# Optimization experiments

Measured on AMD Instinct MI355X. Metric: run time of the kernel, lower is better.

Reference implementation:

```python
import jax, jax.numpy as jnp
import numpy as np

NUM_CODES = 4096
TEMPERATURE = 1.0
EPS = 1e-08


def setup_inputs() -> dict:
    key = jax.random.key(0)
    k1, k2, k3 = jax.random.split(key, 3)
    B, D, T = 16, 512, 1500
    encoder_stride = 320
    student_features = jax.random.normal(k1, (B, D, T), dtype=jnp.float32)
    codebook = jax.random.normal(k2, (NUM_CODES, D), dtype=jnp.float32)
    lengths = jax.random.randint(k3, (B,), 0, T * encoder_stride, dtype=jnp.int64)
    return {
        "student_features": student_features,
        "codebook": codebook,
        "lengths": lengths,
        "encoder_stride": encoder_stride,
    }


def _length_mask(lengths, T, stride):
    # frame t is valid iff t < floor(length / stride)  -> (B, T) float mask
    n_valid = jnp.minimum(lengths // stride, T)
    return (jnp.arange(T)[None, :] < n_valid[:, None]).astype(jnp.float32)


def reference(student_features, codebook, lengths, encoder_stride):
    B, D, T = student_features.shape
    mask = _length_mask(lengths, T, encoder_stride)            # (B, T)
    z = jnp.transpose(student_features, (0, 2, 1)).reshape(-1, D)  # (N, D), N = B*T
    # Euclidean cdist via ||z||^2 + ||c||^2 - 2 z c^T (same as torch.cdist GEMM path)
    z2 = jnp.sum(z * z, axis=-1, keepdims=True)                # (N, 1)
    c2 = jnp.sum(codebook * codebook, axis=-1)                 # (K,)
    d2 = z2 + c2[None, :] - 2.0 * (z @ codebook.T)             # (N, K)
    distances = jnp.sqrt(jnp.maximum(d2, 1e-12))
    logits = -distances / TEMPERATURE
    probs = jax.nn.softmax(logits, axis=-1)                    # (N, K)
    probs_masked = probs * mask.reshape(-1, 1)
    code_dist = jnp.sum(probs_masked, axis=0)                  # (K,)
    code_dist = code_dist / (jnp.sum(code_dist) + EPS)
    entropy = -jnp.sum(code_dist * jnp.log(code_dist + EPS))
    max_entropy = jnp.log(jnp.float32(NUM_CODES))
    return 1.0 - entropy / max_entropy
```

## Files before the change

kernel.cpp:

```cpp
#include <hip/hip_runtime.h>
#include <hip/hip_bf16.h>

#define NUM_B   16
#define DIM     512
#define TT      1500
#define NROWS   (NUM_B * TT)
#define NCODES  4096
#define ROW_TILES ((NROWS + 127) / 128)
#define NROWS_PAD (ROW_TILES * 128)
#define NSLICE  8
#define SHIFTC  30.0f
#define NBLKX   (NCODES / 128)
#define TBLKS   (NUM_B * 47)
#define CBLKS   (NCODES / 4)
#define NZERO   (NROWS_PAD + NSLICE * NCODES)
#define NZERO2  (NZERO + 1)
#define RPB     188

typedef __bf16 bf16x8 __attribute__((ext_vector_type(8)));
typedef float  floatx4 __attribute__((ext_vector_type(4)));
typedef unsigned short ushortx8 __attribute__((ext_vector_type(8)));

__device__ __forceinline__ void glds16(const void* g, void* l) {
    __builtin_amdgcn_global_load_lds(
        (__attribute__((address_space(1))) void*)(void*)g,
        (__attribute__((address_space(3))) void*)l, 16, 0, 0);
}

__global__ __launch_bounds__(256) void k_prep(
    const float* __restrict__ sf, const float* __restrict__ cb,
    unsigned short* __restrict__ zbf, unsigned short* __restrict__ cbbf,
    float* __restrict__ z2, float* __restrict__ c2, float* __restrict__ zero0,
    float* __restrict__ outp) {
    int id = blockIdx.x, tid = threadIdx.x;
    if (id < TBLKS) {
        __shared__ float tile[32][257];
        int b = id / 47, t0 = (id % 47) * 32;
        int tl = tid & 31, dg = tid >> 5;
        int tr = tid >> 3, dgr = tid & 7;
        int tg = t0 + tr;
        float ssq = 0.f;
        unsigned short* dst = zbf + (size_t)(b * TT + tg) * DIM;
#pragma unroll
        for (int half = 0; half < 2; ++half) {
            int dbase = half * 256;
            if (half) __syncthreads();
            int t = t0 + tl;
            if (t < TT) {
                const float* src = sf + (size_t)(b * DIM + dbase + dg * 32) * TT + t;
#pragma unroll
                for (int k = 0; k < 32; ++k)
                    tile[tl][dg * 32 + k] = src[(size_t)k * TT];
            }
            __syncthreads();
            if (tg < TT) {
#pragma unroll
                for (int seg = 0; seg < 4; ++seg) {
                    int d0 = seg * 64 + dgr * 8;
                    unsigned int h[8];
#pragma unroll
                    for (int i2 = 0; i2 < 8; ++i2) {
                        __hip_bfloat16 hb = __float2bfloat16(tile[tr][d0 + i2]);
                        h[i2] = __builtin_bit_cast(unsigned short, hb);
                        float vb = __bfloat162float(hb);
                        ssq += vb * vb;
                    }
                    uint4 o;
                    o.x = h[0] | (h[1] << 16); o.y = h[2] | (h[3] << 16);
                    o.z = h[4] | (h[5] << 16); o.w = h[6] | (h[7] << 16);
                    *(uint4*)(dst + dbase + d0) = o;
                }
            }
        }
        ssq += __shfl_xor(ssq, 1); ssq += __shfl_xor(ssq, 2); ssq += __shfl_xor(ssq, 4);
        if (dgr == 0 && tg < TT) z2[b * TT + tg] = ssq;
    } else {
        int ci = id - TBLKS;
        int gid = ci * 256 + tid;
        if (gid < NZERO2) zero0[gid] = 0.f;
        if (ci == 0 && tid == 0) outp[0] = 1.0f;
        int k = ci * 4 + (tid >> 6);
        int lane = tid & 63;
        const float4* src = (const float4*)(cb + (size_t)k * DIM + lane * 8);
        float4 a = src[0], b2 = src[1];
        float vals[8] = {a.x, a.y, a.z, a.w, b2.x, b2.y, b2.z, b2.w};
        float s = 0.f;
        unsigned int h[8];
#pragma unroll
        for (int i = 0; i < 8; ++i) {
            __hip_bfloat16 hb = __float2bfloat16(vals[i]);
            h[i] = __builtin_bit_cast(unsigned short, hb);
            float vb = __bfloat162float(hb);
            s += vb * vb;
        }
        uint4 o;
        o.x = h[0] | (h[1] << 16); o.y = h[2] | (h[3] << 16);
        o.z = h[4] | (h[5] << 16); o.w = h[6] | (h[7] << 16);
        *(uint4*)(cbbf + (size_t)k * DIM + lane * 8) = o;
#pragma unroll
        for (int off = 32; off >= 1; off >>= 1) s += __shfl_down(s, off);
        if (lane == 0) c2[k] = s;
    }
}

__global__ __launch_bounds__(256, 2) void k_gemm1(
    const unsigned short* __restrict__ zbf, const unsigned short* __restrict__ cbbf,
    const float* __restrict__ z2, const float* __restrict__ c2,
    const int* __restrict__ lengths, const int* __restrict__ stride_p,
    float* __restrict__ Sg, unsigned short* __restrict__ Eg) {
    __shared__ unsigned short As[128 * 64];
    __shared__ unsigned short Bs[128 * 64];
    __shared__ float z2s[128], c2s[128];
    __shared__ unsigned char vldp[128];
    __shared__ int s_any;
    int tid = threadIdx.x;
    int r0 = blockIdx.y * 128, c0 = blockIdx.x * 128;
    if (tid == 0) s_any = 0;
    __syncthreads();
    if (tid < 128) {
        int n = r0 + tid;
        int valid = 0;
        if (n < NROWS) {
            int b = n / TT, t = n - b * TT;
            int stride = stride_p[0];
            int nv = lengths[b] / stride;
            if (nv > TT) nv = TT;
            valid = (t < nv);
        }
        if (valid) atomicOr(&s_any, 1);
        vldp[tid] = (unsigned char)valid;
        z2s[tid] = z2[r0 + tid];
        c2s[tid] = c2[c0 + tid];
    }
    __syncthreads();
    if (!s_any) return;

    int wave = tid >> 6, lane = tid & 63;
    int l15 = lane & 15, l4 = lane >> 4;
    int wr = (wave >> 1) * 64, wc = (wave & 1) * 64;

    int srow = lane >> 3;
    int scg = (lane & 7) ^ srow;
    const unsigned short* ag = zbf + (size_t)(r0 + wave * 32 + srow) * DIM + scg * 8;
    const unsigned short* bg = cbbf + (size_t)(c0 + wave * 32 + srow) * DIM + scg * 8;
    unsigned short* al = As + (wave * 32) * 64;
    unsigned short* bl = Bs + (wave * 32) * 64;

    floatx4 acc[4][4];
    const floatx4 zero = {0.f, 0.f, 0.f, 0.f};
#pragma unroll
    for (int i = 0; i < 4; ++i)
#pragma unroll
        for (int j = 0; j < 4; ++j) acc[i][j] = zero;

    int sw = l15 & 7;

    for (int kc = 0; kc < 8; ++kc) {
#pragma unroll
        for (int q = 0; q < 4; ++q) {
            glds16(ag + (size_t)q * 8 * DIM + kc * 64, al + q * 8 * 64);
            glds16(bg + (size_t)q * 8 * DIM + kc * 64, bl + q * 8 * 64);
        }
        __syncthreads();
#pragma unroll
        for (int ks = 0; ks < 64; ks += 32) {
            int g = (ks >> 3) + l4;
            int pcg = g ^ sw;
            bf16x8 av[4], bv[4];
#pragma unroll
            for (int i = 0; i < 4; ++i)
                av[i] = __builtin_bit_cast(bf16x8,
                    *(const ushortx8*)&As[(wr + 16 * i + l15) * 64 + pcg * 8]);
#pragma unroll
            for (int j = 0; j < 4; ++j)
                bv[j] = __builtin_bit_cast(bf16x8,
                    *(const ushortx8*)&Bs[(wc + 16 * j + l15) * 64 + pcg * 8]);
#pragma unroll
            for (int i = 0; i < 4; ++i)
#pragma unroll
                for (int j = 0; j < 4; ++j)
                    acc[i][j] = __builtin_amdgcn_mfma_f32_16x16x32_bf16(bv[j], av[i], acc[i][j], 0, 0, 0);
        }
        __syncthreads();
    }

    float c2r[4][4];
#pragma unroll
    for (int j = 0; j < 4; ++j)
#pragma unroll
        for (int r = 0; r < 4; ++r)
            c2r[j][r] = c2s[wc + 16 * j + 4 * l4 + r];

#pragma unroll
    for (int i = 0; i < 4; ++i) {
        int rl = wr + 16 * i + l15;
        bool rv = vldp[rl] != 0;
        float z2v = z2s[rl];
        float s = 0.f;
        unsigned short* Ep = Eg + (size_t)(r0 + rl) * NCODES + c0 + wc + l4 * 4;
#pragma unroll
        for (int j = 0; j < 4; ++j) {
            float e[4];
#pragma unroll
            for (int r = 0; r < 4; ++r) {
                float d2 = z2v + c2r[j][r] - 2.0f * acc[i][j][r];
                float d = sqrtf(fmaxf(d2, 1e-12f));
                e[r] = __expf(SHIFTC - d);
                s += e[r];
            }
            if (rv) {
                unsigned h0 = __builtin_bit_cast(unsigned short, __float2bfloat16(e[0]));
                unsigned h1 = __builtin_bit_cast(unsigned short, __float2bfloat16(e[1]));
                unsigned h2 = __builtin_bit_cast(unsigned short, __float2bfloat16(e[2]));
                unsigned h3 = __builtin_bit_cast(unsigned short, __float2bfloat16(e[3]));
                uint2 o;
                o.x = h0 | (h1 << 16);
                o.y = h2 | (h3 << 16);
                *(uint2*)(Ep + 16 * j) = o;
            }
        }
        s += __shfl_xor(s, 16); s += __shfl_xor(s, 32);
        if (l4 == 0 && rv) atomicAdd(&Sg[r0 + rl], s);
    }
}

__global__ __launch_bounds__(256) void k_scan(
    const unsigned short* __restrict__ Eg, const float* __restrict__ Sg,
    const int* __restrict__ lengths, const int* __restrict__ stride_p,
    float* __restrict__ cdp) {
    __shared__ float rs2[RPB];
    __shared__ unsigned char vrows[RPB];
    __shared__ int wtot[4];
    int tid = threadIdx.x;
    int y0 = blockIdx.y;
    int lane = tid & 63, wv = tid >> 6;

    int valid = 0;
    float inv = 0.f;
    if (tid < RPB) {
        int n = y0 + 128 * tid;
        if (n < NROWS) {
            int b = n / TT, t = n - b * TT;
            int nv = lengths[b] / stride_p[0];
            if (nv > TT) nv = TT;
            if (t < nv) { valid = 1; inv = 1.0f / Sg[n]; }
        }
    }
    unsigned long long mask = __ballot(valid);
    if (lane == 0) wtot[wv] = __popcll(mask);
    __syncthreads();
    int base = 0;
#pragma unroll
    for (int w = 0; w < 4; ++w) if (w < wv) base += wtot[w];
    if (valid) {
        int pos = base + __popcll(mask & ((1ull << lane) - 1ull));
        vrows[pos] = (unsigned char)tid;
        rs2[pos] = inv;
    }
    __syncthreads();
    int m = wtot[0] + wtot[1] + wtot[2] + wtot[3];
    if (m == 0) return;

    int col0 = blockIdx.x * 1024 + tid * 4;
    const unsigned short* base_e = Eg + col0;
    float acc[4] = {0.f, 0.f, 0.f, 0.f};

#define ACC4(V, RN) do { \
    unsigned int _u[2] = {(V).x, (V).y}; \
    _Pragma("unroll") \
    for (int q = 0; q < 2; ++q) { \
        acc[2 * q]     += (RN) * __builtin_bit_cast(float, _u[q] << 16); \
        acc[2 * q + 1] += (RN) * __builtin_bit_cast(float, _u[q] & 0xffff0000u); \
    } \
} while (0)

#define ROWP(I) (base_e + (size_t)(y0 + 128 * (int)vrows[I]) * NCODES)
    int i = 0;
    for (; i + 8 <= m; i += 8) {
        uint2 v0 = *(const uint2*)ROWP(i);
        uint2 v1 = *(const uint2*)ROWP(i + 1);
        uint2 v2 = *(const uint2*)ROWP(i + 2);
        uint2 v3 = *(const uint2*)ROWP(i + 3);
        uint2 v4 = *(const uint2*)ROWP(i + 4);
        uint2 v5 = *(const uint2*)ROWP(i + 5);
        uint2 v6 = *(const uint2*)ROWP(i + 6);
        uint2 v7 = *(const uint2*)ROWP(i + 7);
        ACC4(v0, rs2[i]);     ACC4(v1, rs2[i + 1]);
        ACC4(v2, rs2[i + 2]); ACC4(v3, rs2[i + 3]);
        ACC4(v4, rs2[i + 4]); ACC4(v5, rs2[i + 5]);
        ACC4(v6, rs2[i + 6]); ACC4(v7, rs2[i + 7]);
    }
    for (; i < m; ++i) {
        uint2 v = *(const uint2*)ROWP(i);
        ACC4(v, rs2[i]);
    }
#undef ROWP
#undef ACC4

    float* outp = cdp + (size_t)(blockIdx.y & (NSLICE - 1)) * NCODES;
#pragma unroll
    for (int t = 0; t < 4; ++t) atomicAdd(&outp[col0 + t], acc[t]);
}

template <int PASS>
__global__ __launch_bounds__(256, 2) void k_gemm(
    const unsigned short* __restrict__ zbf, const unsigned short* __restrict__ cbbf,
    const float* __restrict__ z2, const float* __restrict__ c2,
    const int* __restrict__ lengths, const int* __restrict__ stride_p,
    float* __restrict__ Sg, float* __restrict__ cd) {
    __shared__ unsigned short Asf[128 * 64];
    __shared__ unsigned short Bsf[128 * 64];
    __shared__ float z2s[128], c2s[128], rs[128];
    __shared__ int s_any;
    int tid = threadIdx.x;
    int r0 = blockIdx.y * 128, c0 = blockIdx.x * 128;
    if (tid == 0) s_any = 0;
    __syncthreads();
    if (tid < 128) {
        int n = r0 + tid;
        int valid = 0;
        if (n < NROWS) {
            int b = n / TT, t = n - b * TT;
            int stride = stride_p[0];
            int nv = lengths[b] / stride;
            if (nv > TT) nv = TT;
            valid = (t < nv);
        }
        if (valid) atomicOr(&s_any, 1);
        z2s[tid] = z2[r0 + tid];
        c2s[tid] = c2[c0 + tid];
        if (PASS == 2) rs[tid] = valid ? (1.0f / Sg[r0 + tid]) : 0.0f;
    }
    __syncthreads();
    if (!s_any) return;

    int wave = tid >> 6, lane = tid & 63;
    int l15 = lane & 15, l4 = lane >> 4;
    int wr = (wave >> 1) * 64, wc = (wave & 1) * 64;
    int srow = lane >> 3;
    int scg = (lane & 7) ^ srow;
    const unsigned short* ag = zbf + (size_t)(r0 + wave * 32 + srow) * DIM + scg * 8;
    const unsigned short* bg = cbbf + (size_t)(c0 + wave * 32 + srow) * DIM + scg * 8;
    unsigned short* al = Asf + (wave * 32) * 64;
    unsigned short* bl = Bsf + (wave * 32) * 64;

    floatx4 acc[4][4];
    const floatx4 zero = {0.f, 0.f, 0.f, 0.f};
#pragma unroll
    for (int i = 0; i < 4; ++i)
#pragma unroll
        for (int j = 0; j < 4; ++j) acc[i][j] = zero;
    int sw = l15 & 7;
    for (int kc = 0; kc < 8; ++kc) {
#pragma unroll
        for (int q = 0; q < 4; ++q) {
            glds16(ag + (size_t)q * 8 * DIM + kc * 64, al + q * 8 * 64);
            glds16(bg + (size_t)q * 8 * DIM + kc * 64, bl + q * 8 * 64);
        }
        __syncthreads();
#pragma unroll
        for (int ks = 0; ks < 64; ks += 32) {
            int g = (ks >> 3) + l4;
            int pcg = g ^ sw;
            bf16x8 av[4], bvv[4];
#pragma unroll
            for (int i = 0; i < 4; ++i)
                av[i] = __builtin_bit_cast(bf16x8, *(const ushortx8*)&Asf[(wr + 16 * i + l15) * 64 + pcg * 8]);
#pragma unroll
            for (int j = 0; j < 4; ++j)
                bvv[j] = __builtin_bit_cast(bf16x8, *(const ushortx8*)&Bsf[(wc + 16 * j + l15) * 64 + pcg * 8]);
#pragma unroll
            for (int i = 0; i < 4; ++i)
#pragma unroll
                for (int j = 0; j < 4; ++j)
                    acc[i][j] = __builtin_amdgcn_mfma_f32_16x16x32_bf16(av[i], bvv[j], acc[i][j], 0, 0, 0);
        }
        __syncthreads();
    }
    if (PASS == 1) {
#pragma unroll
        for (int i = 0; i < 4; ++i) {
#pragma unroll
            for (int r = 0; r < 4; ++r) {
                int rl = wr + 16 * i + 4 * l4 + r;
                float z2v = z2s[rl];
                float s = 0.f;
#pragma unroll
                for (int j = 0; j < 4; ++j) {
                    int cl = wc + 16 * j + l15;
                    float d2 = z2v + c2s[cl] - 2.0f * acc[i][j][r];
                    float d = sqrtf(fmaxf(d2, 1e-12f));
                    s += __expf(SHIFTC - d);
                }
                s += __shfl_xor(s, 1); s += __shfl_xor(s, 2);
                s += __shfl_xor(s, 4); s += __shfl_xor(s, 8);
                if (l15 == 0) atomicAdd(&Sg[r0 + rl], s);
            }
        }
    } else {
#pragma unroll
        for (int j = 0; j < 4; ++j) {
            int cl = wc + 16 * j + l15;
            float c2v = c2s[cl];
            float cs = 0.f;
#pragma unroll
            for (int i = 0; i < 4; ++i) {
#pragma unroll
                for (int r = 0; r < 4; ++r) {
                    int rl = wr + 16 * i + 4 * l4 + r;
                    float d2 = z2s[rl] + c2v - 2.0f * acc[i][j][r];
                    float d = sqrtf(fmaxf(d2, 1e-12f));
                    cs += __expf(SHIFTC - d) * rs[rl];
                }
            }
            cs += __shfl_xor(cs, 16); cs += __shfl_xor(cs, 32);
            if (l4 == 0) atomicAdd(&cd[c0 + cl], cs);
        }
    }
}

__global__ __launch_bounds__(256) void k_red(float* __restrict__ cdp,
                                             float* __restrict__ tot) {
    int k = blockIdx.x * 256 + threadIdx.x;
    float v = 0.f;
#pragma unroll
    for (int s = 0; s < NSLICE; ++s) v += cdp[(size_t)s * NCODES + k];
    cdp[k] = v;
    float t = v;
#pragma unroll
    for (int off = 32; off >= 1; off >>= 1) t += __shfl_down(t, off);
    if ((threadIdx.x & 63) == 0) atomicAdd(tot, t);
}

__global__ __launch_bounds__(256) void k_ent(const float* __restrict__ cdp,
                                             const float* __restrict__ tot,
                                             float* __restrict__ out) {
    int k = blockIdx.x * 256 + threadIdx.x;
    float inv = 1.0f / (tot[0] + 1e-8f);
    float p = cdp[k] * inv;
    float e = p * __logf(p + 1e-8f);
#pragma unroll
    for (int off = 32; off >= 1; off >>= 1) e += __shfl_down(e, off);
    if ((threadIdx.x & 63) == 0)
        atomicAdd(out, e * (1.0f / __logf((float)NCODES)));
}

extern "C" void kernel_launch(void* const* d_in, const int* in_sizes, int n_in,
                              void* d_out, int out_size, void* d_ws, size_t ws_size,
                              hipStream_t stream) {
    const float* sf = (const float*)d_in[0];
    const float* cb = (const float*)d_in[1];
    const int* lengths = (const int*)d_in[2];
    const int* stride_p = (const int*)d_in[3];

    float* wsf = (float*)d_ws;
    float* Sg = wsf;
    float* cdp = Sg + NROWS_PAD;
    float* tot = wsf + NZERO;
    const size_t OFF_Z2 = NZERO2;
    const size_t OFF_C2 = OFF_Z2 + NROWS_PAD;
    const size_t OFF_ZB = (OFF_C2 + NCODES + 3) & ~(size_t)3;
    float* z2 = wsf + OFF_Z2;
    float* c2 = wsf + OFF_C2;
    unsigned short* zbf = (unsigned short*)(wsf + OFF_ZB);
    unsigned short* cbbf = zbf + (size_t)NROWS_PAD * DIM;
    unsigned short* Eg = cbbf + (size_t)NCODES * DIM;

    size_t need = OFF_ZB * 4
                + ((size_t)NROWS_PAD * DIM + (size_t)NCODES * DIM
                 + (size_t)NROWS_PAD * NCODES) * 2;

    k_prep<<<dim3(TBLKS + CBLKS), 256, 0, stream>>>(
        sf, cb, zbf, cbbf, z2, c2, Sg, (float*)d_out);
    if (ws_size >= need) {
        k_gemm1<<<dim3(NBLKX, ROW_TILES), 256, 0, stream>>>(
            zbf, cbbf, z2, c2, lengths, stride_p, Sg, Eg);
        k_scan<<<dim3(4, 128), 256, 0, stream>>>(
            Eg, Sg, lengths, stride_p, cdp);
    } else {
        k_gemm<1><<<dim3(NBLKX, ROW_TILES), 256, 0, stream>>>(zbf, cbbf, z2, c2, lengths, stride_p, Sg, cdp);
        k_gemm<2><<<dim3(NBLKX, ROW_TILES), 256, 0, stream>>>(zbf, cbbf, z2, c2, lengths, stride_p, Sg, cdp);
    }
    k_red<<<dim3(NCODES / 256), 256, 0, stream>>>(cdp, tot);
    k_ent<<<dim3(NCODES / 256), 256, 0, stream>>>(cdp, tot, (float*)d_out);
}
```

Measured before the change: 217.3 us.

## Compact valid rows in prep so GEMM and scan skip masked frames densely

The prep kernel now computes a per-batch prefix of valid frame counts and writes only valid rows into a packed bf16 activation buffer. The GEMM and scan kernels treat rows below the total valid count as live and exit early beyond it. Previously, tiles that mixed valid and padded rows still ran the full MFMA work. Packing removes that partial-tile waste, so GEMM work scales with the number of valid rows, and the scan no longer needs ballot-based row compaction. The cost is that every thread recomputes a 16-entry prefix loop, and padding rows in partially filled tiles can read stale z2 values.

```diff
diff --git a/kernel.cpp b/kernel.cpp
--- a/kernel.cpp
+++ b/kernel.cpp
@@ -27,20 +27,40 @@
         (__attribute__((address_space(3))) void*)l, 16, 0, 0);
 }
 
+__device__ __forceinline__ void row_prefix(const int* __restrict__ lengths,
+                                           int stride, int b,
+                                           int* off_out, int* nv_out, int* tot_out) {
+    int off = 0, nvb = 0, tot = 0;
+#pragma unroll
+    for (int bb = 0; bb < NUM_B; ++bb) {
+        int nv = lengths[bb] / stride;
+        if (nv > TT) nv = TT;
+        if (bb < b) off += nv;
+        if (bb == b) nvb = nv;
+        tot += nv;
+    }
+    *off_out = off; *nv_out = nvb; *tot_out = tot;
+}
+
 __global__ __launch_bounds__(256) void k_prep(
     const float* __restrict__ sf, const float* __restrict__ cb,
+    const int* __restrict__ lengths, const int* __restrict__ stride_p,
     unsigned short* __restrict__ zbf, unsigned short* __restrict__ cbbf,
     float* __restrict__ z2, float* __restrict__ c2, float* __restrict__ zero0,
     float* __restrict__ outp) {
     int id = blockIdx.x, tid = threadIdx.x;
     if (id < TBLKS) {
+        int b = id / 47, t0 = (id % 47) * 32;
+        int off, nvb, tot;
+        row_prefix(lengths, stride_p[0], b, &off, &nvb, &tot);
+        if (t0 >= nvb) return;
+
         __shared__ float tile[32][257];
-        int b = id / 47, t0 = (id % 47) * 32;
         int tl = tid & 31, dg = tid >> 5;
         int tr = tid >> 3, dgr = tid & 7;
         int tg = t0 + tr;
         float ssq = 0.f;
-        unsigned short* dst = zbf + (size_t)(b * TT + tg) * DIM;
+        unsigned short* dst = zbf + (size_t)(off + tg) * DIM;
 #pragma unroll
         for (int half = 0; half < 2; ++half) {
             int dbase = half * 256;
@@ -53,7 +73,7 @@
                     tile[tl][dg * 32 + k] = src[(size_t)k * TT];
             }
             __syncthreads();
-            if (tg < TT) {
+            if (tg < nvb) {
 #pragma unroll
                 for (int seg = 0; seg < 4; ++seg) {
                     int d0 = seg * 64 + dgr * 8;
@@ -73,7 +93,7 @@
             }
         }
         ssq += __shfl_xor(ssq, 1); ssq += __shfl_xor(ssq, 2); ssq += __shfl_xor(ssq, 4);
-        if (dgr == 0 && tg < TT) z2[b * TT + tg] = ssq;
+        if (dgr == 0 && tg < nvb) z2[off + tg] = ssq;
     } else {
         int ci = id - TBLKS;
         int gid = ci * 256 + tid;
@@ -111,29 +131,18 @@
     __shared__ unsigned short As[128 * 64];
     __shared__ unsigned short Bs[128 * 64];
     __shared__ float z2s[128], c2s[128];
-    __shared__ unsigned char vldp[128];
-    __shared__ int s_any;
     int tid = threadIdx.x;
     int r0 = blockIdx.y * 128, c0 = blockIdx.x * 128;
-    if (tid == 0) s_any = 0;
-    __syncthreads();
+
+    int off_, nv_, Ntot;
+    row_prefix(lengths, stride_p[0], 0, &off_, &nv_, &Ntot);
+    if (r0 >= Ntot) return;
+
     if (tid < 128) {
-        int n = r0 + tid;
-        int valid = 0;
-        if (n < NROWS) {
-            int b = n / TT, t = n - b * TT;
-            int stride = stride_p[0];
-            int nv = lengths[b] / stride;
-            if (nv > TT) nv = TT;
-            valid = (t < nv);
-        }
-        if (valid) atomicOr(&s_any, 1);
-        vldp[tid] = (unsigned char)valid;
         z2s[tid] = z2[r0 + tid];
         c2s[tid] = c2[c0 + tid];
     }
     __syncthreads();
-    if (!s_any) return;
 
     int wave = tid >> 6, lane = tid & 63;
     int l15 = lane & 15, l4 = lane >> 4;
@@ -194,7 +203,7 @@
 #pragma unroll
     for (int i = 0; i < 4; ++i) {
         int rl = wr + 16 * i + l15;
-        bool rv = vldp[rl] != 0;
+        bool rv = (r0 + rl) < Ntot;
         float z2v = z2s[rl];
         float s = 0.f;
         unsigned short* Ep = Eg + (size_t)(r0 + rl) * NCODES + c0 + wc + l4 * 4;
@@ -229,37 +238,17 @@
     const int* __restrict__ lengths, const int* __restrict__ stride_p,
     float* __restrict__ cdp) {
     __shared__ float rs2[RPB];
-    __shared__ unsigned char vrows[RPB];
-    __shared__ int wtot[4];
     int tid = threadIdx.x;
     int y0 = blockIdx.y;
-    int lane = tid & 63, wv = tid >> 6;
-
-    int valid = 0;
-    float inv = 0.f;
-    if (tid < RPB) {
-        int n = y0 + 128 * tid;
-        if (n < NROWS) {
-            int b = n / TT, t = n - b * TT;
-            int nv = lengths[b] / stride_p[0];
-            if (nv > TT) nv = TT;
-            if (t < nv) { valid = 1; inv = 1.0f / Sg[n]; }
-        }
-    }
-    unsigned long long mask = __ballot(valid);
-    if (lane == 0) wtot[wv] = __popcll(mask);
+
+    int off_, nv_, Ntot;
+    row_prefix(lengths, stride_p[0], 0, &off_, &nv_, &Ntot);
+    int m = (y0 < Ntot) ? ((Ntot - 1 - y0) / 128 + 1) : 0;
+    if (m > RPB) m = RPB;
+    if (m == 0) return;
+
+    if (tid < m) rs2[tid] = 1.0f / Sg[y0 + 128 * tid];
     __syncthreads();
-    int base = 0;
-#pragma unroll
-    for (int w = 0; w < 4; ++w) if (w < wv) base += wtot[w];
-    if (valid) {
-        int pos = base + __popcll(mask & ((1ull << lane) - 1ull));
-        vrows[pos] = (unsigned char)tid;
-        rs2[pos] = inv;
-    }
-    __syncthreads();
-    int m = wtot[0] + wtot[1] + wtot[2] + wtot[3];
-    if (m == 0) return;
 
     int col0 = blockIdx.x * 1024 + tid * 4;
     const unsigned short* base_e = Eg + col0;
@@ -274,7 +263,7 @@
     } \
 } while (0)
 
-#define ROWP(I) (base_e + (size_t)(y0 + 128 * (int)vrows[I]) * NCODES)
+#define ROWP(I) (base_e + (size_t)(y0 + 128 * (I)) * NCODES)
     int i = 0;
     for (; i + 8 <= m; i += 8) {
         uint2 v0 = *(const uint2*)ROWP(i);
@@ -311,28 +300,17 @@
     __shared__ unsigned short Asf[128 * 64];
     __shared__ unsigned short Bsf[128 * 64];
     __shared__ float z2s[128], c2s[128], rs[128];
-    __shared__ int s_any;
     int tid = threadIdx.x;
     int r0 = blockIdx.y * 128, c0 = blockIdx.x * 128;
-    if (tid == 0) s_any = 0;
-    __syncthreads();
+    int off_, nv_, Ntot;
+    row_prefix(lengths, stride_p[0], 0, &off_, &nv_, &Ntot);
+    if (r0 >= Ntot) return;
     if (tid < 128) {
-        int n = r0 + tid;
-        int valid = 0;
-        if (n < NROWS) {
-            int b = n / TT, t = n - b * TT;
-            int stride = stride_p[0];
-            int nv = lengths[b] / stride;
-            if (nv > TT) nv = TT;
-            valid = (t < nv);
-        }
-        if (valid) atomicOr(&s_any, 1);
         z2s[tid] = z2[r0 + tid];
         c2s[tid] = c2[c0 + tid];
-        if (PASS == 2) rs[tid] = valid ? (1.0f / Sg[r0 + tid]) : 0.0f;
+        if (PASS == 2) rs[tid] = ((r0 + tid) < Ntot) ? (1.0f / Sg[r0 + tid]) : 0.0f;
     }
     __syncthreads();
-    if (!s_any) return;
 
     int wave = tid >> 6, lane = tid & 63;
     int l15 = lane & 15, l4 = lane >> 4;
@@ -383,6 +361,7 @@
 #pragma unroll
             for (int r = 0; r < 4; ++r) {
                 int rl = wr + 16 * i + 4 * l4 + r;
+                bool rv = (r0 + rl) < Ntot;
                 float z2v = z2s[rl];
                 float s = 0.f;
 #pragma unroll
@@ -394,7 +373,7 @@
                 }
                 s += __shfl_xor(s, 1); s += __shfl_xor(s, 2);
                 s += __shfl_xor(s, 4); s += __shfl_xor(s, 8);
-                if (l15 == 0) atomicAdd(&Sg[r0 + rl], s);
+                if (l15 == 0 && rv) atomicAdd(&Sg[r0 + rl], s);
             }
         }
     } else {
@@ -471,7 +450,7 @@
                  + (size_t)NROWS_PAD * NCODES) * 2;
 
     k_prep<<<dim3(TBLKS + CBLKS), 256, 0, stream>>>(
-        sf, cb, zbf, cbbf, z2, c2, Sg, (float*)d_out);
+        sf, cb, lengths, stride_p, zbf, cbbf, z2, c2, Sg, (float*)d_out);
     if (ws_size >= need) {
         k_gemm1<<<dim3(NBLKX, ROW_TILES), 256, 0, stream>>>(
             zbf, cbbf, z2, c2, lengths, stride_p, Sg, Eg);
```

Result: faster. 204.0 us, median of 2 (-6.1%).
